# Performance work log

Measured on AMD Instinct MI355X. Metric: run time of the kernel, lower is better.

The kernel has to match this reference:

```python
import jax, jax.numpy as jnp
import numpy as np

B = 524288
D_IN = 128
H = 16          # hard-coded by amax slicing in MLSTMCell
D_OUT = 4


def _quant(x, amax):
    # torch quant_tensor: clamp(round(x * 127/amax), -127, 127) -> int8 (kept as
    # integer-valued float32 here; exact since |v| <= 127)
    if amax.ndim > 1:
        amax = jnp.squeeze(amax, 1)
    return jnp.clip(jnp.round(x * (127.0 / amax)), -127.0, 127.0)


def _dequant(x, amax, double=False):
    max_range = 127.0 ** 2 if double else 127.0
    scale = max_range / amax
    if scale.ndim > 1:
        scale = jnp.squeeze(scale, 1)
    return x / scale


def setup_inputs() -> dict:
    key = jax.random.key(0)
    ks = jax.random.split(key, 13)
    # weights are stored pre-quantized int8 (integer-valued); torch casts them
    # to int32 before matmul, so integer-valued float32 is bit-exact in fp32
    intw = lambda k, shp: jax.random.randint(k, shp, -127, 128).astype(jnp.float32)
    x = jax.random.normal(ks[0], (B, D_IN), dtype=jnp.float32)
    h = jax.random.normal(ks[1], (B, H), dtype=jnp.float32) * 0.1
    c = jax.random.normal(ks[2], (B, H), dtype=jnp.float32) * 0.1
    w1 = intw(ks[3], (H, D_IN))          # net.0.weight
    w_ih = intw(ks[4], (4 * H, H))       # lstm.weight_ih
    w_hh = intw(ks[5], (4 * H, H))       # lstm.weight_hh
    w_out = intw(ks[6], (D_OUT, H))      # output_layer.weight
    u = lambda k, shp, lo, hi: jax.random.uniform(k, shp, minval=lo, maxval=hi, dtype=jnp.float32)
    amax_in0 = u(ks[7], (), 1.0, 4.0)            # net.0._input_quantizer._amax (per-tensor)
    amax_w0 = u(ks[8], (H, 1), 32.0, 127.0)      # net.0._weight_quantizer._amax (per-channel)
    amax_lstm_in = u(ks[9], (), 1.0, 4.0)        # lstm._input_quantizer._amax
    amax_w_lstm = u(ks[10], (4 * H, 1), 32.0, 127.0)  # lstm._weight_quantizer._amax
    amax_out_in = u(ks[11], (), 1.0, 4.0)        # output_layer._input_quantizer._amax
    amax_w_out = u(ks[12], (D_OUT, 1), 32.0, 127.0)   # output_layer._weight_quantizer._amax
    return dict(x=x, h=h, c=c, w1=w1, w_ih=w_ih, w_hh=w_hh, w_out=w_out,
                amax_in0=amax_in0, amax_w0=amax_w0, amax_lstm_in=amax_lstm_in,
                amax_w_lstm=amax_w_lstm, amax_out_in=amax_out_in, amax_w_out=amax_w_out)


def reference(x, h, c, w1, w_ih, w_hh, w_out, amax_in0, amax_w0,
              amax_lstm_in, amax_w_lstm, amax_out_in, amax_w_out):
    # --- fc_1: quantize input, int matmul, relu, requantize for lstm ---
    xq = _quant(x, amax_in0)                     # [B, D_IN] int8-valued
    a = xq @ w1.T                                # [B, H] int32-valued (exact in fp32)
    a = jnp.maximum(a, 0.0)                      # relu
    a = _quant(_dequant(a, amax_in0 * amax_w0, double=True), amax_lstm_in)  # [B, H]
    # --- quantize hidden state (hc arrives as float) ---
    hq = _quant(h, amax_lstm_in)
    cq = _quant(c, amax_lstm_in)
    # --- MLSTMCell ---
    amax = amax_lstm_in * amax_w_lstm            # [4H, 1]
    gates = a @ w_ih.T + hq @ w_hh.T             # [B, 4H] int32-valued
    gates = _dequant(gates, amax, double=True)
    i, f, g, o = jnp.split(gates, 4, axis=1)
    gates = jnp.concatenate([jax.nn.sigmoid(i), jax.nn.sigmoid(f),
                             jnp.tanh(g), jax.nn.sigmoid(o)], axis=1)
    gq = _quant(gates, amax)                     # [B, 4H] int8-valued
    i, f, g, o = jnp.split(gq, 4, axis=1)
    cy = (_dequant(f * cq, amax[16:32] * 3.4764, double=True)
          + _dequant(i * g, amax[:16] * amax[32:48], double=True))
    od = _dequant(o, amax[48:], double=False)
    hy = od * jnp.tanh(cy)
    # --- output layer ---
    xo = _quant(hy, amax_out_in) @ w_out.T       # [B, D_OUT]
    xo = _dequant(xo, amax_out_in * amax_w_out, double=True)
    return xo, hy, cy
```

## Files before the change

kernel.cpp:

```cpp
#include <hip/hip_runtime.h>
#include <math.h>
#include <limits.h>


#define OFF_QS    0
#define OFF_SFC1  4
#define OFF_SG    20
#define OFF_QG    84
#define OFF_SCF   148
#define OFF_SCIG  164
#define OFF_SOD   180
#define OFF_SXO   196
#define OFF_VBG   200
#define OFF_TI    216
#define OFF_TF    280
#define OFF_TO    344
#define OFF_TG    408
#define OFF_IGT   536
#define OFF_ODT   1064
#define OFF_W1P   1192
#define OFF_WIHP  1704
#define OFF_WHHP  1960
#define OFF_WOUTP 2216

__device__ __forceinline__ float qclip(float v) {
    return fminf(fmaxf(v, -127.0f), 127.0f);
}

__device__ __forceinline__ int sdot4(int a, int b, int c) {
#if __has_builtin(__builtin_amdgcn_sdot4)
    return __builtin_amdgcn_sdot4(a, b, c, false);
#else
    c += ((a << 24) >> 24) * ((b << 24) >> 24);
    c += ((a << 16) >> 24) * ((b << 16) >> 24);
    c += ((a << 8)  >> 24) * ((b << 8)  >> 24);
    c += (a >> 24) * (b >> 24);
    return c;
#endif
}

__device__ __forceinline__ int pack4i(int a, int b, int c, int d) {
    return (a & 255) | ((b & 255) << 8) | ((c & 255) << 16) | (d << 24);
}

__device__ __forceinline__ int pack4f(const float* p) {
    return pack4i((int)p[0], (int)p[1], (int)p[2], (int)p[3]);
}

typedef __attribute__((address_space(1))) const void g_void;
typedef __attribute__((address_space(3))) void l_void;

__device__ __forceinline__ void stage16(const float* g, float* l) {
    __builtin_amdgcn_global_load_lds((g_void*)g, (l_void*)l, 16, 0, 0);
}

#define WAIT_VM0()   { asm volatile("s_waitcnt vmcnt(0)" ::: "memory"); __builtin_amdgcn_sched_barrier(0); }
#define WAIT_LGKM0() { asm volatile("s_waitcnt lgkmcnt(0)" ::: "memory"); __builtin_amdgcn_sched_barrier(0); }

__device__ __forceinline__ int qeval_sig(int gi, float s, float q) {
    float v = (float)gi / s;
    float a = 1.0f / (1.0f + expf(-v));
    return (int)qclip(rintf(a * q));
}
__device__ __forceinline__ int qeval_tanh(int gi, float s, float q) {
    float v = (float)gi / s;
    float a = tanhf(v);
    return (int)qclip(rintf(a * q));
}

#define GLIM 1048576

__device__ int search_thr_sig(float s, float q, int target) {
    if (qeval_sig(GLIM, s, q) < target) return INT_MAX;
    int lo = -GLIM, hi = GLIM;
    while (hi - lo > 1) {
        int mid = lo + ((hi - lo) >> 1);
        if (qeval_sig(mid, s, q) >= target) hi = mid; else lo = mid;
    }
    return hi;
}
__device__ int search_thr_tanh(float s, float q, int target) {
    if (qeval_tanh(GLIM, s, q) < target) return INT_MAX;
    int lo = -GLIM, hi = GLIM;
    while (hi - lo > 1) {
        int mid = lo + ((hi - lo) >> 1);
        if (qeval_tanh(mid, s, q) >= target) hi = mid; else lo = mid;
    }
    return hi;
}

__global__ void __launch_bounds__(256) setup_scales(
    const float* __restrict__ w1, const float* __restrict__ w_ih,
    const float* __restrict__ w_hh, const float* __restrict__ w_out,
    const float* __restrict__ a_in0, const float* __restrict__ a_w0,
    const float* __restrict__ a_lstm, const float* __restrict__ a_wl,
    const float* __restrict__ a_out, const float* __restrict__ a_wo,
    float* __restrict__ wsf)
{
    int t = threadIdx.x;
    int* wsi = (int*)wsf;
    const float amax_in0 = a_in0[0], amax_lstm = a_lstm[0], amax_out = a_out[0];
    if (t == 0) {
        wsf[OFF_QS + 0] = 127.0f / amax_in0;
        wsf[OFF_QS + 1] = 127.0f / amax_lstm;
        wsf[OFF_QS + 2] = 127.0f / amax_out;
    }
    if (t < 16) wsf[OFF_SFC1 + t] = 16129.0f / (amax_in0 * a_w0[t]);
    if (t < 64) {
        float am = amax_lstm * a_wl[t];
        wsf[OFF_SG + t] = 16129.0f / am;
        wsf[OFF_QG + t] = 127.0f / am;
    }
    if (t < 16) {
        float amf = amax_lstm * a_wl[16 + t];
        wsf[OFF_SCF + t] = 16129.0f / (amf * 3.4764f);
        float ami = amax_lstm * a_wl[t];
        float amg = amax_lstm * a_wl[32 + t];
        wsf[OFF_SCIG + t] = 16129.0f / (ami * amg);
        float amo = amax_lstm * a_wl[48 + t];
        wsf[OFF_SOD + t] = 127.0f / amo;
    }
    if (t < 4) wsf[OFF_SXO + t] = 16129.0f / (amax_out * a_wo[t]);
    if (t < 16) {
        float am = amax_lstm * a_wl[32 + t];
        float s = 16129.0f / am, q = 127.0f / am;
        wsi[OFF_VBG + t] = qeval_tanh(-GLIM, s, q);
    }
    for (int i = t; i < 512; i += 256) wsi[OFF_W1P + i]  = pack4f(w1 + 4 * i);
    for (int i = t; i < 256; i += 256) wsi[OFF_WIHP + i] = pack4f(w_ih + 4 * i);
    for (int i = t; i < 256; i += 256) wsi[OFF_WHHP + i] = pack4f(w_hh + 4 * i);
    if (t < 16) wsi[OFF_WOUTP + t] = pack4f(w_out + 4 * t);
}

__global__ void __launch_bounds__(256) setup_tables(float* __restrict__ wsf)
{
    int gtid = blockIdx.x * 256 + threadIdx.x;
    int* wsi = (int*)wsf;
    if (gtid < 64) {
        int m = gtid >> 2, k = gtid & 3;
        wsi[OFF_TI + gtid] = search_thr_sig(wsf[OFF_SG + m], wsf[OFF_QG + m], k + 1);
    } else if (gtid < 128) {
        int u = gtid - 64, m = u >> 2, k = u & 3;
        wsi[OFF_TF + u] = search_thr_sig(wsf[OFF_SG + 16 + m], wsf[OFF_QG + 16 + m], k + 1);
    } else if (gtid < 192) {
        int u = gtid - 128, m = u >> 2, k = u & 3;
        wsi[OFF_TO + u] = search_thr_sig(wsf[OFF_SG + 48 + m], wsf[OFF_QG + 48 + m], k + 1);
    } else if (gtid < 320) {
        int u = gtid - 192, m = u >> 3, k = u & 7;
        int target = wsi[OFF_VBG + m] + 1 + k;
        wsi[OFF_TG + u] = search_thr_tanh(wsf[OFF_SG + 32 + m], wsf[OFF_QG + 32 + m], target);
    } else if (gtid < 848) {
        int u = gtid - 320, m = u / 33, p = u % 33;
        wsf[OFF_IGT + u] = (float)(p - 16) / wsf[OFF_SCIG + m];
    } else if (gtid < 928) {
        int u = gtid - 848, m = u / 5, oq = u % 5;
        wsf[OFF_ODT + m * 8 + oq] = (float)oq / wsf[OFF_SOD + m];
    }
}

__global__ void __launch_bounds__(256) mlpq_kernel(
    const float* __restrict__ x, const float* __restrict__ h, const float* __restrict__ c,
    const float* __restrict__ wsf,
    float* __restrict__ out_xo, float* __restrict__ out_hy, float* __restrict__ out_cy,
    int nrows)
{
    __shared__ float s_tab[656];
    __shared__ __align__(1024) float s_stage[4][1024];

    for (int i = threadIdx.x; i < 656; i += 256) s_tab[i] = wsf[OFF_IGT + i];
    __syncthreads();
    const float* s_igt = s_tab;
    const float* s_odt = s_tab + 528;

    const int tid = threadIdx.x;
    const int wv  = tid >> 6;
    const int rl  = tid & 63;
    const int wrow0 = blockIdx.x * 256 + wv * 64;
    const int r = wrow0 + rl;

    const int sw = (rl >> 1) & 3;
    const int qs_stage = (rl & 3) ^ ((rl >> 3) & 3);
    const int rstage = wrow0 + (rl >> 2);

    float* buf = &s_stage[wv][0];
    const float4* buf4 = reinterpret_cast<const float4*>(buf);

    const int* __restrict__ wsi = (const int*)wsf;
    const float qs_in   = wsf[OFF_QS + 0];
    const float qs_lstm = wsf[OFF_QS + 1];
    const float qs_out  = wsf[OFF_QS + 2];

    const float* gph = h + (size_t)rstage * 16 + qs_stage * 4;
    const float* gpc = c + (size_t)rstage * 16 + qs_stage * 4;
    const float* gpx = x + (size_t)rstage * 128 + qs_stage * 4;

    stage16(gph + 0 * 256, buf + 0 * 256);
    stage16(gph + 1 * 256, buf + 1 * 256);
    stage16(gph + 2 * 256, buf + 2 * 256);
    stage16(gph + 3 * 256, buf + 3 * 256);
    WAIT_VM0();
    int hql[4];
#pragma unroll
    for (int q = 0; q < 4; ++q) {
        float4 v = buf4[rl * 4 + (q ^ sw)];
        hql[q] = pack4i((int)qclip(rintf(v.x * qs_lstm)),
                        (int)qclip(rintf(v.y * qs_lstm)),
                        (int)qclip(rintf(v.z * qs_lstm)),
                        (int)qclip(rintf(v.w * qs_lstm)));
    }
    WAIT_LGKM0();

    int acc[16];
#pragma unroll
    for (int j = 0; j < 16; ++j) acc[j] = 0;

    stage16(gpx + 0 * 2048, buf + 0 * 256);
    stage16(gpx + 1 * 2048, buf + 1 * 256);
    stage16(gpx + 2 * 2048, buf + 2 * 256);
    stage16(gpx + 3 * 2048, buf + 3 * 256);

#pragma unroll
    for (int kc = 0; kc < 8; ++kc) {
        WAIT_VM0();
        float4 xv[4];
#pragma unroll
        for (int q = 0; q < 4; ++q) xv[q] = buf4[rl * 4 + (q ^ sw)];
        WAIT_LGKM0();
        if (kc < 7) {
            const float* g = gpx + (kc + 1) * 16;
            stage16(g + 0 * 2048, buf + 0 * 256);
            stage16(g + 1 * 2048, buf + 1 * 256);
            stage16(g + 2 * 2048, buf + 2 * 256);
            stage16(g + 3 * 2048, buf + 3 * 256);
        } else {
            stage16(gpc + 0 * 256, buf + 0 * 256);
            stage16(gpc + 1 * 256, buf + 1 * 256);
            stage16(gpc + 2 * 256, buf + 2 * 256);
            stage16(gpc + 3 * 256, buf + 3 * 256);
        }
#pragma unroll
        for (int q = 0; q < 4; ++q) {
            float4 v = xv[q];
            int w = pack4i((int)qclip(rintf(v.x * qs_in)),
                           (int)qclip(rintf(v.y * qs_in)),
                           (int)qclip(rintf(v.z * qs_in)),
                           (int)qclip(rintf(v.w * qs_in)));
#pragma unroll
            for (int j = 0; j < 16; ++j)
                acc[j] = sdot4(w, wsi[OFF_W1P + j * 32 + kc * 4 + q], acc[j]);
        }
    }

    int aql[4];
#pragma unroll
    for (int jg = 0; jg < 4; ++jg) {
        int q[4];
#pragma unroll
        for (int u = 0; u < 4; ++u) {
            int j = jg * 4 + u;
            int ai = acc[j] > 0 ? acc[j] : 0;
            float dq = (float)ai / wsf[OFF_SFC1 + j];
            q[u] = (int)qclip(rintf(dq * qs_lstm));
        }
        aql[jg] = pack4i(q[0], q[1], q[2], q[3]);
    }

    WAIT_VM0();

    float hyv[16], cyv[16];
    int xqi[16];

#pragma unroll
    for (int mg = 0; mg < 4; ++mg) {
        float4 cv = buf4[rl * 4 + (mg ^ sw)];
        float cvals[4] = {cv.x, cv.y, cv.z, cv.w};
#pragma unroll
        for (int t = 0; t < 4; ++t) {
            const int m = mg * 4 + t;
            int gi = 0, gf = 0, gg = 0, go = 0;
#pragma unroll
            for (int p = 0; p < 4; ++p) {
                int ap = aql[p], hp = hql[p];
                gi = sdot4(ap, wsi[OFF_WIHP + (m)      * 4 + p], gi);
                gi = sdot4(hp, wsi[OFF_WHHP + (m)      * 4 + p], gi);
                gf = sdot4(ap, wsi[OFF_WIHP + (m + 16) * 4 + p], gf);
                gf = sdot4(hp, wsi[OFF_WHHP + (m + 16) * 4 + p], gf);
                gg = sdot4(ap, wsi[OFF_WIHP + (m + 32) * 4 + p], gg);
                gg = sdot4(hp, wsi[OFF_WHHP + (m + 32) * 4 + p], gg);
                go = sdot4(ap, wsi[OFF_WIHP + (m + 48) * 4 + p], go);
                go = sdot4(hp, wsi[OFF_WHHP + (m + 48) * 4 + p], go);
            }
            int iq = (gi >= wsi[OFF_TI + m * 4 + 0]) + (gi >= wsi[OFF_TI + m * 4 + 1])
                   + (gi >= wsi[OFF_TI + m * 4 + 2]) + (gi >= wsi[OFF_TI + m * 4 + 3]);
            int fq = (gf >= wsi[OFF_TF + m * 4 + 0]) + (gf >= wsi[OFF_TF + m * 4 + 1])
                   + (gf >= wsi[OFF_TF + m * 4 + 2]) + (gf >= wsi[OFF_TF + m * 4 + 3]);
            int oq = (go >= wsi[OFF_TO + m * 4 + 0]) + (go >= wsi[OFF_TO + m * 4 + 1])
                   + (go >= wsi[OFF_TO + m * 4 + 2]) + (go >= wsi[OFF_TO + m * 4 + 3]);
            int gq = wsi[OFF_VBG + m]
                   + (gg >= wsi[OFF_TG + m * 8 + 0]) + (gg >= wsi[OFF_TG + m * 8 + 1])
                   + (gg >= wsi[OFF_TG + m * 8 + 2]) + (gg >= wsi[OFF_TG + m * 8 + 3])
                   + (gg >= wsi[OFF_TG + m * 8 + 4]) + (gg >= wsi[OFF_TG + m * 8 + 5])
                   + (gg >= wsi[OFF_TG + m * 8 + 6]) + (gg >= wsi[OFF_TG + m * 8 + 7]);

            int cqv = (int)qclip(rintf(cvals[t] * qs_lstm));

            float cy = (float)(fq * cqv) / wsf[OFF_SCF + m]
                     + s_igt[m * 33 + (iq * gq + 16)];
            float od = s_odt[m * 8 + oq];
            float hy = od * tanhf(cy);

            hyv[m] = hy;
            cyv[m] = cy;
            xqi[m] = (int)qclip(rintf(hy * qs_out));
        }
    }

    int xql[4];
#pragma unroll
    for (int p = 0; p < 4; ++p)
        xql[p] = pack4i(xqi[p * 4], xqi[p * 4 + 1], xqi[p * 4 + 2], xqi[p * 4 + 3]);

    float4 xov;
    {
        int s0 = 0, s1 = 0, s2 = 0, s3 = 0;
#pragma unroll
        for (int p = 0; p < 4; ++p) {
            s0 = sdot4(xql[p], wsi[OFF_WOUTP + 0 * 4 + p], s0);
            s1 = sdot4(xql[p], wsi[OFF_WOUTP + 1 * 4 + p], s1);
            s2 = sdot4(xql[p], wsi[OFF_WOUTP + 2 * 4 + p], s2);
            s3 = sdot4(xql[p], wsi[OFF_WOUTP + 3 * 4 + p], s3);
        }
        xov.x = (float)s0 / wsf[OFF_SXO + 0];
        xov.y = (float)s1 / wsf[OFF_SXO + 1];
        xov.z = (float)s2 / wsf[OFF_SXO + 2];
        xov.w = (float)s3 / wsf[OFF_SXO + 3];
    }

    float4* __restrict__ hyrow = reinterpret_cast<float4*>(out_hy) + (size_t)r * 4;
    float4* __restrict__ cyrow = reinterpret_cast<float4*>(out_cy) + (size_t)r * 4;
#pragma unroll
    for (int mg = 0; mg < 4; ++mg)
        hyrow[mg] = make_float4(hyv[mg * 4], hyv[mg * 4 + 1], hyv[mg * 4 + 2], hyv[mg * 4 + 3]);
#pragma unroll
    for (int mg = 0; mg < 4; ++mg)
        cyrow[mg] = make_float4(cyv[mg * 4], cyv[mg * 4 + 1], cyv[mg * 4 + 2], cyv[mg * 4 + 3]);
    reinterpret_cast<float4*>(out_xo)[r] = xov;
}

extern "C" void kernel_launch(void* const* d_in, const int* in_sizes, int n_in,
                              void* d_out, int out_size, void* d_ws, size_t ws_size,
                              hipStream_t stream) {
    const float* x      = (const float*)d_in[0];
    const float* h      = (const float*)d_in[1];
    const float* c      = (const float*)d_in[2];
    const float* w1     = (const float*)d_in[3];
    const float* w_ih   = (const float*)d_in[4];
    const float* w_hh   = (const float*)d_in[5];
    const float* w_out  = (const float*)d_in[6];
    const float* a_in0  = (const float*)d_in[7];
    const float* a_w0   = (const float*)d_in[8];
    const float* a_lstm = (const float*)d_in[9];
    const float* a_wl   = (const float*)d_in[10];
    const float* a_out  = (const float*)d_in[11];
    const float* a_wo   = (const float*)d_in[12];

    const int B = in_sizes[0] / 128;
    float* out    = (float*)d_out;
    float* out_xo = out;
    float* out_hy = out + (size_t)B * 4;
    float* out_cy = out + (size_t)B * 20;
    float* wsf    = (float*)d_ws;

    hipLaunchKernelGGL(setup_scales, dim3(1), dim3(256), 0, stream,
                       w1, w_ih, w_hh, w_out, a_in0, a_w0, a_lstm, a_wl, a_out, a_wo, wsf);
    hipLaunchKernelGGL(setup_tables, dim3(4), dim3(256), 0, stream, wsf);

    dim3 block(256);
    dim3 grid((B + 255) / 256);
    hipLaunchKernelGGL(mlpq_kernel, grid, block, 0, stream,
                       x, h, c, wsf, out_xo, out_hy, out_cy, B);
}
```

Before: 115.5 us.

## Double-buffer LDS staging of x chunks and merge setup kernels into one

Merges the two setup kernels into a single 1024-thread launch that recomputes the scales it needs locally instead of reading them back from the workspace. In the main kernel, a second LDS buffer per wave lets the loads for the next two x chunks be in flight at once, waiting with vmcnt(4) instead of vmcnt(0), so global latency overlaps with the dot-product work. This doubles per-block LDS use, which may reduce occupancy, and the hand-counted vmcnt waits have to match the order in which loads are issued.

New measurement: 109.0 us. 1.06x faster.

```diff
diff --git a/kernel.cpp b/kernel.cpp
--- a/kernel.cpp
+++ b/kernel.cpp
@@ -55,6 +55,7 @@
 }
 
 #define WAIT_VM0()   { asm volatile("s_waitcnt vmcnt(0)" ::: "memory"); __builtin_amdgcn_sched_barrier(0); }
+#define WAIT_VM4()   { asm volatile("s_waitcnt vmcnt(4)" ::: "memory"); __builtin_amdgcn_sched_barrier(0); }
 #define WAIT_LGKM0() { asm volatile("s_waitcnt lgkmcnt(0)" ::: "memory"); __builtin_amdgcn_sched_barrier(0); }
 
 __device__ __forceinline__ int qeval_sig(int gi, float s, float q) {
@@ -89,7 +90,7 @@
     return hi;
 }
 
-__global__ void __launch_bounds__(256) setup_scales(
+__global__ void __launch_bounds__(1024) setup_all(
     const float* __restrict__ w1, const float* __restrict__ w_ih,
     const float* __restrict__ w_hh, const float* __restrict__ w_out,
     const float* __restrict__ a_in0, const float* __restrict__ a_w0,
@@ -97,9 +98,10 @@
     const float* __restrict__ a_out, const float* __restrict__ a_wo,
     float* __restrict__ wsf)
 {
-    int t = threadIdx.x;
+    const int t = threadIdx.x;
     int* wsi = (int*)wsf;
     const float amax_in0 = a_in0[0], amax_lstm = a_lstm[0], amax_out = a_out[0];
+
     if (t == 0) {
         wsf[OFF_QS + 0] = 127.0f / amax_in0;
         wsf[OFF_QS + 1] = 127.0f / amax_lstm;
@@ -114,47 +116,50 @@
     if (t < 16) {
         float amf = amax_lstm * a_wl[16 + t];
         wsf[OFF_SCF + t] = 16129.0f / (amf * 3.4764f);
+        float amo = amax_lstm * a_wl[48 + t];
+        wsf[OFF_SOD + t] = 127.0f / amo;
         float ami = amax_lstm * a_wl[t];
         float amg = amax_lstm * a_wl[32 + t];
         wsf[OFF_SCIG + t] = 16129.0f / (ami * amg);
-        float amo = amax_lstm * a_wl[48 + t];
-        wsf[OFF_SOD + t] = 127.0f / amo;
+        float s = 16129.0f / amg, q = 127.0f / amg;
+        wsi[OFF_VBG + t] = qeval_tanh(-GLIM, s, q);
     }
     if (t < 4) wsf[OFF_SXO + t] = 16129.0f / (amax_out * a_wo[t]);
-    if (t < 16) {
-        float am = amax_lstm * a_wl[32 + t];
+
+    if (t < 512) wsi[OFF_W1P + t]  = pack4f(w1 + 4 * t);
+    if (t < 256) { wsi[OFF_WIHP + t] = pack4f(w_ih + 4 * t);
+                   wsi[OFF_WHHP + t] = pack4f(w_hh + 4 * t); }
+    if (t < 16)  wsi[OFF_WOUTP + t] = pack4f(w_out + 4 * t);
+
+    if (t < 64) {
+        int m = t >> 2, k = t & 3;
+        float am = amax_lstm * a_wl[m];
+        wsi[OFF_TI + t] = search_thr_sig(16129.0f / am, 127.0f / am, k + 1);
+    } else if (t < 128) {
+        int u = t - 64, m = u >> 2, k = u & 3;
+        float am = amax_lstm * a_wl[16 + m];
+        wsi[OFF_TF + u] = search_thr_sig(16129.0f / am, 127.0f / am, k + 1);
+    } else if (t < 192) {
+        int u = t - 128, m = u >> 2, k = u & 3;
+        float am = amax_lstm * a_wl[48 + m];
+        wsi[OFF_TO + u] = search_thr_sig(16129.0f / am, 127.0f / am, k + 1);
+    } else if (t < 320) {
+        int u = t - 192, m = u >> 3, k = u & 7;
+        float am = amax_lstm * a_wl[32 + m];
         float s = 16129.0f / am, q = 127.0f / am;
-        wsi[OFF_VBG + t] = qeval_tanh(-GLIM, s, q);
-    }
-    for (int i = t; i < 512; i += 256) wsi[OFF_W1P + i]  = pack4f(w1 + 4 * i);
-    for (int i = t; i < 256; i += 256) wsi[OFF_WIHP + i] = pack4f(w_ih + 4 * i);
-    for (int i = t; i < 256; i += 256) wsi[OFF_WHHP + i] = pack4f(w_hh + 4 * i);
-    if (t < 16) wsi[OFF_WOUTP + t] = pack4f(w_out + 4 * t);
-}
-
-__global__ void __launch_bounds__(256) setup_tables(float* __restrict__ wsf)
-{
-    int gtid = blockIdx.x * 256 + threadIdx.x;
-    int* wsi = (int*)wsf;
-    if (gtid < 64) {
-        int m = gtid >> 2, k = gtid & 3;
-        wsi[OFF_TI + gtid] = search_thr_sig(wsf[OFF_SG + m], wsf[OFF_QG + m], k + 1);
-    } else if (gtid < 128) {
-        int u = gtid - 64, m = u >> 2, k = u & 3;
-        wsi[OFF_TF + u] = search_thr_sig(wsf[OFF_SG + 16 + m], wsf[OFF_QG + 16 + m], k + 1);
-    } else if (gtid < 192) {
-        int u = gtid - 128, m = u >> 2, k = u & 3;
-        wsi[OFF_TO + u] = search_thr_sig(wsf[OFF_SG + 48 + m], wsf[OFF_QG + 48 + m], k + 1);
-    } else if (gtid < 320) {
-        int u = gtid - 192, m = u >> 3, k = u & 7;
-        int target = wsi[OFF_VBG + m] + 1 + k;
-        wsi[OFF_TG + u] = search_thr_tanh(wsf[OFF_SG + 32 + m], wsf[OFF_QG + 32 + m], target);
-    } else if (gtid < 848) {
-        int u = gtid - 320, m = u / 33, p = u % 33;
-        wsf[OFF_IGT + u] = (float)(p - 16) / wsf[OFF_SCIG + m];
-    } else if (gtid < 928) {
-        int u = gtid - 848, m = u / 5, oq = u % 5;
-        wsf[OFF_ODT + m * 8 + oq] = (float)oq / wsf[OFF_SOD + m];
+        int vb = qeval_tanh(-GLIM, s, q);
+        wsi[OFF_TG + u] = search_thr_tanh(s, q, vb + 1 + k);
+    } else if (t < 848) {
+        int u = t - 320, m = u / 33, p = u % 33;
+        float ami = amax_lstm * a_wl[m];
+        float amg = amax_lstm * a_wl[32 + m];
+        float scig = 16129.0f / (ami * amg);
+        wsf[OFF_IGT + u] = (float)(p - 16) / scig;
+    } else if (t < 928) {
+        int u = t - 848, m = u / 5, oq = u % 5;
+        float amo = amax_lstm * a_wl[48 + m];
+        float sod = 127.0f / amo;
+        wsf[OFF_ODT + m * 8 + oq] = (float)oq / sod;
     }
 }
 
@@ -165,7 +170,7 @@
     int nrows)
 {
     __shared__ float s_tab[656];
-    __shared__ __align__(1024) float s_stage[4][1024];
+    __shared__ __align__(1024) float s_stage[4][2048];
 
     for (int i = threadIdx.x; i < 656; i += 256) s_tab[i] = wsf[OFF_IGT + i];
     __syncthreads();
@@ -182,8 +187,8 @@
     const int qs_stage = (rl & 3) ^ ((rl >> 3) & 3);
     const int rstage = wrow0 + (rl >> 2);
 
-    float* buf = &s_stage[wv][0];
-    const float4* buf4 = reinterpret_cast<const float4*>(buf);
+    float* bufE = &s_stage[wv][0];
+    float* bufO = &s_stage[wv][1024];
 
     const int* __restrict__ wsi = (const int*)wsf;
     const float qs_in   = wsf[OFF_QS + 0];
@@ -194,49 +199,64 @@
     const float* gpc = c + (size_t)rstage * 16 + qs_stage * 4;
     const float* gpx = x + (size_t)rstage * 128 + qs_stage * 4;
 
-    stage16(gph + 0 * 256, buf + 0 * 256);
-    stage16(gph + 1 * 256, buf + 1 * 256);
-    stage16(gph + 2 * 256, buf + 2 * 256);
-    stage16(gph + 3 * 256, buf + 3 * 256);
-    WAIT_VM0();
+    stage16(gph + 0 * 256, bufO + 0 * 256);
+    stage16(gph + 1 * 256, bufO + 1 * 256);
+    stage16(gph + 2 * 256, bufO + 2 * 256);
+    stage16(gph + 3 * 256, bufO + 3 * 256);
+    stage16(gpx + 0 * 2048, bufE + 0 * 256);
+    stage16(gpx + 1 * 2048, bufE + 1 * 256);
+    stage16(gpx + 2 * 2048, bufE + 2 * 256);
+    stage16(gpx + 3 * 2048, bufE + 3 * 256);
+
+    WAIT_VM4();
+    float4 hv[4];
+    {
+        const float4* b4 = reinterpret_cast<const float4*>(bufO);
+#pragma unroll
+        for (int q = 0; q < 4; ++q) hv[q] = b4[rl * 4 + (q ^ sw)];
+    }
+    WAIT_LGKM0();
+    {
+        const float* g = gpx + 1 * 16;
+        stage16(g + 0 * 2048, bufO + 0 * 256);
+        stage16(g + 1 * 2048, bufO + 1 * 256);
+        stage16(g + 2 * 2048, bufO + 2 * 256);
+        stage16(g + 3 * 2048, bufO + 3 * 256);
+    }
     int hql[4];
 #pragma unroll
     for (int q = 0; q < 4; ++q) {
-        float4 v = buf4[rl * 4 + (q ^ sw)];
+        float4 v = hv[q];
         hql[q] = pack4i((int)qclip(rintf(v.x * qs_lstm)),
                         (int)qclip(rintf(v.y * qs_lstm)),
                         (int)qclip(rintf(v.z * qs_lstm)),
                         (int)qclip(rintf(v.w * qs_lstm)));
     }
-    WAIT_LGKM0();
 
     int acc[16];
 #pragma unroll
     for (int j = 0; j < 16; ++j) acc[j] = 0;
 
-    stage16(gpx + 0 * 2048, buf + 0 * 256);
-    stage16(gpx + 1 * 2048, buf + 1 * 256);
-    stage16(gpx + 2 * 2048, buf + 2 * 256);
-    stage16(gpx + 3 * 2048, buf + 3 * 256);
-
 #pragma unroll
     for (int kc = 0; kc < 8; ++kc) {
-        WAIT_VM0();
+        WAIT_VM4();
+        float* bk = (kc & 1) ? bufO : bufE;
+        const float4* b4 = reinterpret_cast<const float4*>(bk);
         float4 xv[4];
 #pragma unroll
-        for (int q = 0; q < 4; ++q) xv[q] = buf4[rl * 4 + (q ^ sw)];
+        for (int q = 0; q < 4; ++q) xv[q] = b4[rl * 4 + (q ^ sw)];
         WAIT_LGKM0();
-        if (kc < 7) {
-            const float* g = gpx + (kc + 1) * 16;
-            stage16(g + 0 * 2048, buf + 0 * 256);
-            stage16(g + 1 * 2048, buf + 1 * 256);
-            stage16(g + 2 * 2048, buf + 2 * 256);
-            stage16(g + 3 * 2048, buf + 3 * 256);
-        } else {
-            stage16(gpc + 0 * 256, buf + 0 * 256);
-            stage16(gpc + 1 * 256, buf + 1 * 256);
-            stage16(gpc + 2 * 256, buf + 2 * 256);
-            stage16(gpc + 3 * 256, buf + 3 * 256);
+        if (kc <= 5) {
+            const float* g = gpx + (kc + 2) * 16;
+            stage16(g + 0 * 2048, bk + 0 * 256);
+            stage16(g + 1 * 2048, bk + 1 * 256);
+            stage16(g + 2 * 2048, bk + 2 * 256);
+            stage16(g + 3 * 2048, bk + 3 * 256);
+        } else if (kc == 6) {
+            stage16(gpc + 0 * 256, bk + 0 * 256);
+            stage16(gpc + 1 * 256, bk + 1 * 256);
+            stage16(gpc + 2 * 256, bk + 2 * 256);
+            stage16(gpc + 3 * 256, bk + 3 * 256);
         }
 #pragma unroll
         for (int q = 0; q < 4; ++q) {
@@ -267,12 +287,13 @@
 
     WAIT_VM0();
 
+    const float4* c4 = reinterpret_cast<const float4*>(bufE);
     float hyv[16], cyv[16];
     int xqi[16];
 
 #pragma unroll
     for (int mg = 0; mg < 4; ++mg) {
-        float4 cv = buf4[rl * 4 + (mg ^ sw)];
+        float4 cv = c4[rl * 4 + (mg ^ sw)];
         float cvals[4] = {cv.x, cv.y, cv.z, cv.w};
 #pragma unroll
         for (int t = 0; t < 4; ++t) {
@@ -371,9 +392,8 @@
     float* out_cy = out + (size_t)B * 20;
     float* wsf    = (float*)d_ws;
 
-    hipLaunchKernelGGL(setup_scales, dim3(1), dim3(256), 0, stream,
+    hipLaunchKernelGGL(setup_all, dim3(1), dim3(1024), 0, stream,
                        w1, w_ih, w_hh, w_out, a_in0, a_w0, a_lstm, a_wl, a_out, a_wo, wsf);
-    hipLaunchKernelGGL(setup_tables, dim3(4), dim3(256), 0, stream, wsf);
 
     dim3 block(256);
     dim3 grid((B + 255) / 256);
```
